# Performance work log

Hardware: AMD Instinct MI355X
Metric: run time of the kernel (lower is better)

The kernel has to match this reference:

```python
import jax, jax.numpy as jnp
import numpy as np

CANVAS = 28
MARGIN = 2
HALF = CANVAS / 2.0          # 14
SCALE = CANVAS / 2.0 - MARGIN  # 12
P = 2        # num_paths
SEG = 4      # final segments
T = 8        # curve samples per bezier segment
AA = 2       # 2x2 = 4 anti-alias subsamples per pixel


def _lin(x, w, b):
    return x @ w + b


def _render(cp, widths, alphas):
    """diffvg-style rasterizer.
    cp: [B,P,S,4,2] cubic bezier control points, widths/alphas: [B,P].
    Returns [B,1,H,W] image over white background (paths paint dark).
    """
    B = cp.shape[0]
    t = jnp.linspace(0.0, 1.0, T)
    mt = 1.0 - t
    basis = jnp.stack([mt**3, 3*mt**2*t, 3*mt*t**2, t**3], axis=1)  # [T,4]
    pts = jnp.einsum('tk,bpskd->bpstd', basis, cp)                   # [B,P,S,T,2]
    q = pts.reshape(B, P, SEG * T, 2)                                # polyline [B,P,M,2]

    # 2x2 subpixel sample grid over the canvas
    Nf = CANVAS * AA
    c = (jnp.arange(Nf, dtype=jnp.float32) + 0.5) / AA               # fine coords
    sy, sx = jnp.meshgrid(c, c, indexing='ij')
    s = jnp.stack([sx.ravel(), sy.ravel()], axis=-1)                 # [Ns,2] (x,y)

    # stroke coverage: distance from each sample to nearest curve sample
    qq = jnp.sum(q * q, axis=-1)                                     # [B,P,M]
    ss = jnp.sum(s * s, axis=-1)                                     # [Ns]
    cr = jnp.einsum('bpmd,nd->bpmn', q, s)                           # [B,P,M,Ns]
    d2 = jnp.maximum(qq[..., None] + ss - 2.0 * cr, 0.0)
    dist = jnp.sqrt(jnp.min(d2, axis=2))                             # [B,P,Ns]
    stroke = jnp.clip(widths[..., None] * 0.5 + 0.5 - dist, 0.0, 1.0)

    # fill coverage: even-odd crossing number on the closed polyline
    qn = jnp.roll(q, -1, axis=2)
    x0, y0 = q[..., 0], q[..., 1]
    x1, y1 = qn[..., 0], qn[..., 1]
    syf, sxf = s[:, 1], s[:, 0]
    crossing_band = (y0[..., None] > syf) != (y1[..., None] > syf)   # [B,P,M,Ns]
    te = (syf - y0[..., None]) / (y1[..., None] - y0[..., None] + 1e-8)
    xint = x0[..., None] + te * (x1 - x0)[..., None]
    ncross = jnp.sum((crossing_band & (sxf < xint)).astype(jnp.int32), axis=2)
    inside = (ncross % 2).astype(dist.dtype)                         # [B,P,Ns]

    cov = jnp.maximum(inside, stroke)
    img = jnp.prod(1.0 - alphas[..., None] * cov, axis=1)            # composite over paths, bg=1
    img = img.reshape(B, CANVAS, AA, CANVAS, AA).mean(axis=(2, 4))   # AA resolve
    return img[:, None]                                              # [B,1,H,W]


def setup_inputs() -> dict:
    key = jax.random.key(0)
    ks = jax.random.split(key, 16)
    def W(k, i, o):
        return jax.random.normal(k, (i, o), jnp.float32) / np.sqrt(i).astype(np.float32)
    B = 128
    return {
        'x': jax.random.uniform(ks[0], (B, 1, 28, 28), jnp.float32),
        'eps': jax.random.normal(ks[1], (B, 64), jnp.float32),
        'enc_w1': W(ks[2], 784, 256), 'enc_b1': jnp.zeros((256,), jnp.float32),
        'enc_w2': W(ks[3], 256, 256), 'enc_b2': jnp.zeros((256,), jnp.float32),
        'mu_w': W(ks[4], 256, 64), 'mu_b': jnp.zeros((64,), jnp.float32),
        'lv_w': W(ks[5], 256, 64), 'lv_b': jnp.zeros((64,), jnp.float32),
        'dec_w1': W(ks[6], 64, 512), 'dec_b1': jnp.zeros((512,), jnp.float32),
        'dec_w2': W(ks[7], 512, 512), 'dec_b2': jnp.zeros((512,), jnp.float32),
        'cp_w': W(ks[8], 512, 28), 'cp_b': jnp.zeros((28,), jnp.float32),
        'ref_w1': W(ks[9], 92, 512), 'ref_b1': jnp.zeros((512,), jnp.float32),
        'ref_w2': W(ks[10], 512, 52), 'ref_b2': jnp.zeros((52,), jnp.float32),
        'wd_w': W(ks[11], 512, 2), 'wd_b': jnp.zeros((2,), jnp.float32),
        'al_w': W(ks[12], 512, 2), 'al_b': jnp.zeros((2,), jnp.float32),
    }


def reference(x, eps, enc_w1, enc_b1, enc_w2, enc_b2, mu_w, mu_b, lv_w, lv_b,
              dec_w1, dec_b1, dec_w2, dec_b2, cp_w, cp_b,
              ref_w1, ref_b1, ref_w2, ref_b2, wd_w, wd_b, al_w, al_b):
    B = x.shape[0]
    # encoder
    h = jax.nn.leaky_relu(_lin(x.reshape(B, -1), enc_w1, enc_b1), 0.2)
    h = jax.nn.leaky_relu(_lin(h, enc_w2, enc_b2), 0.2)
    mu = _lin(h, mu_w, mu_b)
    logvar = _lin(h, lv_w, lv_b)
    z = mu + eps * jnp.exp(0.5 * logvar)
    # hierarchical decoder
    h2 = jax.nn.selu(_lin(jax.nn.selu(_lin(z, dec_w1, dec_b1)), dec_w2, dec_b2))
    coarse = jnp.tanh(_lin(h2, cp_w, cp_b)).reshape(B, P, 7, 2) * SCALE + HALF
    pts_norm = (coarse - HALF) / SCALE
    h_in = jnp.concatenate([z, pts_norm.reshape(B, -1)], axis=-1)
    refined = jnp.tanh(_lin(jax.nn.selu(_lin(h_in, ref_w1, ref_b1)), ref_w2, ref_b2))
    points = refined.reshape(B, P, 13, 2) * SCALE + HALF
    seg_idx = 3 * jnp.arange(SEG)[:, None] + jnp.arange(4)[None, :]  # [S,4]
    control_points = points[:, :, seg_idx, :]                         # [B,P,S,4,2]
    widths = jax.nn.sigmoid(_lin(h2, wd_w, wd_b)) * 2.0 + 1.0
    alphas = jax.nn.sigmoid(_lin(h2, al_w, al_b))
    rendered = 1.0 - _render(control_points, widths, alphas)          # white digit on black
    return (rendered, mu, logvar, control_points, widths, alphas)
```

## Files before the change

kernel.cpp:

```cpp
#include <hip/hip_runtime.h>
#include <math.h>


#define O_MU  100352
#define O_LV  108544
#define O_CP  116736
#define O_WD  124928
#define O_AL  125184

__device__ __forceinline__ float leaky(float x) {
    return x >= 0.0f ? x : 0.2f * x;
}
__device__ __forceinline__ float selu(float x) {
    const float scale = 1.0507009873554805f;
    const float alpha = 1.6732632423543772f;
    return x > 0.0f ? scale * x : scale * (alpha * expm1f(x));
}
__device__ __forceinline__ void fma4(float4& acc, float a, const float4 w) {
    acc.x = fmaf(a, w.x, acc.x);
    acc.y = fmaf(a, w.y, acc.y);
    acc.z = fmaf(a, w.z, acc.z);
    acc.w = fmaf(a, w.w, acc.w);
}
__device__ __forceinline__ void add4(float4& a, const float4 b) {
    a.x += b.x; a.y += b.y; a.z += b.z; a.w += b.w;
}

__global__ __launch_bounds__(512, 1)
void pipeline(const float* __restrict__ x, const float* __restrict__ eps,
              const float* __restrict__ enc_w1, const float* __restrict__ enc_b1,
              const float* __restrict__ enc_w2, const float* __restrict__ enc_b2,
              const float* __restrict__ mu_w, const float* __restrict__ mu_b,
              const float* __restrict__ lv_w, const float* __restrict__ lv_b,
              const float* __restrict__ dec_w1, const float* __restrict__ dec_b1,
              const float* __restrict__ dec_w2, const float* __restrict__ dec_b2,
              const float* __restrict__ cp_w, const float* __restrict__ cp_b,
              const float* __restrict__ ref_w1, const float* __restrict__ ref_b1,
              const float* __restrict__ ref_w2, const float* __restrict__ ref_b2,
              const float* __restrict__ wd_w, const float* __restrict__ wd_b,
              const float* __restrict__ al_w, const float* __restrict__ al_b,
              float* __restrict__ out) {
    __shared__ float  sX[784];
    __shared__ float4 sPart4[512];
    __shared__ float  sH1[256];
    __shared__ float  sHe[256];
    __shared__ float  sML[128];
    __shared__ float  sIn[96];
    __shared__ float  sD1[512];
    __shared__ float  sH2[512];
    __shared__ float  sR1[512];
    __shared__ float  sP[56];
    __shared__ float  sQ[128];
    __shared__ float  sWA[4];

    const int row = blockIdx.x;
    const int tid = threadIdx.x;

    for (int i = tid; i < 784; i += 512) sX[i] = x[row * 784 + i];
    __syncthreads();

    {
        const int jv = tid & 63, g = tid >> 6;
        const float4* __restrict__ W4 = (const float4*)enc_w1;
        const int k0 = g * 98;
        float4 acc0 = {0,0,0,0}, acc1 = {0,0,0,0};
#pragma unroll 7
        for (int i = 0; i < 98; i += 2) {
            fma4(acc0, sX[k0 + i + 0], W4[(k0 + i + 0) * 64 + jv]);
            fma4(acc1, sX[k0 + i + 1], W4[(k0 + i + 1) * 64 + jv]);
        }
        add4(acc0, acc1);
        sPart4[g * 64 + jv] = acc0;
    }
    __syncthreads();
    if (tid < 64) {
        float4 s = ((const float4*)enc_b1)[tid];
#pragma unroll
        for (int g = 0; g < 8; g++) add4(s, sPart4[g * 64 + tid]);
        s.x = leaky(s.x); s.y = leaky(s.y); s.z = leaky(s.z); s.w = leaky(s.w);
        ((float4*)sH1)[tid] = s;
    }
    __syncthreads();

    {
        const int jv = tid & 63, g = tid >> 6;
        const float4* __restrict__ W4 = (const float4*)enc_w2;
        const int k0 = g * 32;
        float4 acc0 = {0,0,0,0}, acc1 = {0,0,0,0};
#pragma unroll 8
        for (int i = 0; i < 32; i += 2) {
            fma4(acc0, sH1[k0 + i + 0], W4[(k0 + i + 0) * 64 + jv]);
            fma4(acc1, sH1[k0 + i + 1], W4[(k0 + i + 1) * 64 + jv]);
        }
        add4(acc0, acc1);
        sPart4[g * 64 + jv] = acc0;
    }
    __syncthreads();
    if (tid < 64) {
        float4 s = ((const float4*)enc_b2)[tid];
#pragma unroll
        for (int g = 0; g < 8; g++) add4(s, sPart4[g * 64 + tid]);
        s.x = leaky(s.x); s.y = leaky(s.y); s.z = leaky(s.z); s.w = leaky(s.w);
        ((float4*)sHe)[tid] = s;
    }
    __syncthreads();

    {
        const int o4 = tid >> 4, g = tid & 15;
        const int jv = o4 & 15;
        const float4* __restrict__ W4 = (const float4*)(o4 < 16 ? mu_w : lv_w);
        const int k0 = g * 16;
        float4 acc = {0,0,0,0};
#pragma unroll
        for (int i = 0; i < 16; i++)
            fma4(acc, sHe[k0 + i], W4[(k0 + i) * 16 + jv]);
        sPart4[o4 * 16 + g] = acc;
    }
    __syncthreads();
    if (tid < 32) {
        const int jv = tid & 15;
        float4 s = (tid < 16) ? ((const float4*)mu_b)[jv] : ((const float4*)lv_b)[jv];
#pragma unroll
        for (int g = 0; g < 16; g++) add4(s, sPart4[tid * 16 + g]);
        ((float4*)sML)[tid] = s;
        float4* o4p = (float4*)(out + (tid < 16 ? O_MU : O_LV) + row * 64);
        o4p[jv] = s;
    }
    __syncthreads();
    if (tid < 64)
        sIn[tid] = fmaf(eps[row * 64 + tid], expf(0.5f * sML[64 + tid]), sML[tid]);
    __syncthreads();

    {
        const int jv = tid & 127, g = tid >> 7;
        const float4* __restrict__ W4 = (const float4*)dec_w1;
        const int k0 = g * 16;
        float4 acc = {0,0,0,0};
#pragma unroll
        for (int i = 0; i < 16; i++)
            fma4(acc, sIn[k0 + i], W4[(k0 + i) * 128 + jv]);
        sPart4[g * 128 + jv] = acc;
    }
    __syncthreads();
    if (tid < 128) {
        float4 s = ((const float4*)dec_b1)[tid];
#pragma unroll
        for (int g = 0; g < 4; g++) add4(s, sPart4[g * 128 + tid]);
        s.x = selu(s.x); s.y = selu(s.y); s.z = selu(s.z); s.w = selu(s.w);
        ((float4*)sD1)[tid] = s;
    }
    __syncthreads();

    {
        const int jv = tid & 127, g = tid >> 7;
        const float4* __restrict__ W4 = (const float4*)dec_w2;
        const int k0 = g * 128;
        float4 acc0 = {0,0,0,0}, acc1 = {0,0,0,0};
        float4 acc2 = {0,0,0,0}, acc3 = {0,0,0,0};
#pragma unroll 4
        for (int i = 0; i < 128; i += 4) {
            fma4(acc0, sD1[k0 + i + 0], W4[(k0 + i + 0) * 128 + jv]);
            fma4(acc1, sD1[k0 + i + 1], W4[(k0 + i + 1) * 128 + jv]);
            fma4(acc2, sD1[k0 + i + 2], W4[(k0 + i + 2) * 128 + jv]);
            fma4(acc3, sD1[k0 + i + 3], W4[(k0 + i + 3) * 128 + jv]);
        }
        add4(acc0, acc1); add4(acc2, acc3); add4(acc0, acc2);
        sPart4[g * 128 + jv] = acc0;
    }
    __syncthreads();
    if (tid < 128) {
        float4 s = ((const float4*)dec_b2)[tid];
#pragma unroll
        for (int g = 0; g < 4; g++) add4(s, sPart4[g * 128 + tid]);
        s.x = selu(s.x); s.y = selu(s.y); s.z = selu(s.z); s.w = selu(s.w);
        ((float4*)sH2)[tid] = s;
    }
    __syncthreads();

    {
        const int o = tid >> 4, g = tid & 15;
        const float* __restrict__ W;
        int ldw, col;
        if (o < 28)      { W = cp_w; ldw = 28; col = o; }
        else if (o < 30) { W = wd_w; ldw = 2;  col = o - 28; }
        else             { W = al_w; ldw = 2;  col = o - 30; }
        float acc = 0.f;
        for (int k = g; k < 512; k += 16) acc = fmaf(sH2[k], W[k * ldw + col], acc);
        acc += __shfl_xor(acc, 1);
        acc += __shfl_xor(acc, 2);
        acc += __shfl_xor(acc, 4);
        acc += __shfl_xor(acc, 8);
        if (g == 0) {
            if (o < 28) {
                sIn[64 + o] = tanhf(acc + cp_b[col]);
            } else if (o < 30) {
                float v = 1.f / (1.f + expf(-(acc + wd_b[col])));
                v = fmaf(v, 2.f, 1.f);
                out[O_WD + row * 2 + col] = v;
                sWA[col] = v;
            } else {
                float v = 1.f / (1.f + expf(-(acc + al_b[col])));
                out[O_AL + row * 2 + col] = v;
                sWA[2 + col] = v;
            }
        }
    }
    __syncthreads();

    {
        const int jv = tid & 127, g = tid >> 7;
        const float4* __restrict__ W4 = (const float4*)ref_w1;
        const int k0 = g * 23;
        float4 acc = {0,0,0,0};
#pragma unroll
        for (int i = 0; i < 23; i++)
            fma4(acc, sIn[k0 + i], W4[(k0 + i) * 128 + jv]);
        sPart4[g * 128 + jv] = acc;
    }
    __syncthreads();
    if (tid < 128) {
        float4 s = ((const float4*)ref_b1)[tid];
#pragma unroll
        for (int g = 0; g < 4; g++) add4(s, sPart4[g * 128 + tid]);
        s.x = selu(s.x); s.y = selu(s.y); s.z = selu(s.z); s.w = selu(s.w);
        ((float4*)sR1)[tid] = s;
    }
    __syncthreads();

    {
        const int o = tid >> 3, g = tid & 7;
        float acc = 0.f;
        if (o < 52)
            for (int k = g; k < 512; k += 8) acc = fmaf(sR1[k], ref_w2[k * 52 + o], acc);
        acc += __shfl_xor(acc, 1);
        acc += __shfl_xor(acc, 2);
        acc += __shfl_xor(acc, 4);
        if (g == 0 && o < 52)
            sP[o] = fmaf(tanhf(acc + ref_b2[o]), 12.f, 14.f);
    }
    __syncthreads();

    if (tid < 64) {
        int idx = tid;
        int p = idx >> 5, rest = idx & 31;
        int s = rest >> 3, kk = (rest >> 1) & 3, d = idx & 1;
        out[O_CP + row * 64 + idx] = sP[p * 26 + (3 * s + kk) * 2 + d];
    }
    if (tid < 128) {
        int idx = tid;
        int p = idx >> 6, s = (idx >> 4) & 3, ti = (idx >> 1) & 7, d = idx & 1;
        float t = (float)ti / 7.0f;
        float mt = 1.0f - t;
        float c0 = mt * mt * mt;
        float c1 = 3.f * mt * mt * t;
        float c2 = 3.f * mt * t * t;
        float c3 = t * t * t;
        const float* base = sP + p * 26 + (3 * s) * 2 + d;
        sQ[idx] = c0 * base[0] + c1 * base[2] + c2 * base[4] + c3 * base[6];
    }
    __syncthreads();

    const float2* __restrict__ sQ2 = (const float2*)sQ;
    for (int u = tid; u < 3136; u += 512) {
        const int pixel = u >> 2;
        const int sub = u & 3;
        const int py = pixel / 28;
        const int px = pixel - py * 28;
        const float sy = ((float)(2 * py + (sub >> 1)) + 0.5f) * 0.5f;
        const float sx = ((float)(2 * px + (sub & 1)) + 0.5f) * 0.5f;
        float img = 1.0f;
#pragma unroll
        for (int p = 0; p < 2; p++) {
            float dmin2 = 1e30f;
            int cnt = 0;
            float2 cur = sQ2[p * 32];
            bool bp = cur.y > sy;
#pragma unroll
            for (int m = 0; m < 32; m++) {
                float2 nxt = sQ2[p * 32 + ((m + 1) & 31)];
                float dx = sx - cur.x;
                float dy = sy - cur.y;
                dmin2 = fminf(dmin2, fmaf(dx, dx, dy * dy));
                bool bn = nxt.y > sy;
                float den = nxt.y - cur.y + 1e-8f;
                float lhs = dx * den;
                float rhs = dy * (nxt.x - cur.x);
                if ((bp != bn) && ((lhs < rhs) == (den > 0.0f))) cnt++;
                cur = nxt;
                bp = bn;
            }
            float dist = sqrtf(dmin2);
            float stroke = fminf(fmaxf(fmaf(sWA[p], 0.5f, 0.5f) - dist, 0.f), 1.f);
            float cov = fmaxf((float)(cnt & 1), stroke);
            img *= fmaf(-sWA[2 + p], cov, 1.0f);
        }
        img += __shfl_xor(img, 1);
        img += __shfl_xor(img, 2);
        if (sub == 0) out[row * 784 + pixel] = 1.0f - 0.25f * img;
    }
}

extern "C" void kernel_launch(void* const* d_in, const int* in_sizes, int n_in,
                              void* d_out, int out_size, void* d_ws, size_t ws_size,
                              hipStream_t stream) {
    const float* x      = (const float*)d_in[0];
    const float* eps    = (const float*)d_in[1];
    const float* enc_w1 = (const float*)d_in[2];
    const float* enc_b1 = (const float*)d_in[3];
    const float* enc_w2 = (const float*)d_in[4];
    const float* enc_b2 = (const float*)d_in[5];
    const float* mu_w   = (const float*)d_in[6];
    const float* mu_b   = (const float*)d_in[7];
    const float* lv_w   = (const float*)d_in[8];
    const float* lv_b   = (const float*)d_in[9];
    const float* dec_w1 = (const float*)d_in[10];
    const float* dec_b1 = (const float*)d_in[11];
    const float* dec_w2 = (const float*)d_in[12];
    const float* dec_b2 = (const float*)d_in[13];
    const float* cp_w   = (const float*)d_in[14];
    const float* cp_b   = (const float*)d_in[15];
    const float* ref_w1 = (const float*)d_in[16];
    const float* ref_b1 = (const float*)d_in[17];
    const float* ref_w2 = (const float*)d_in[18];
    const float* ref_b2 = (const float*)d_in[19];
    const float* wd_w   = (const float*)d_in[20];
    const float* wd_b   = (const float*)d_in[21];
    const float* al_w   = (const float*)d_in[22];
    const float* al_b   = (const float*)d_in[23];

    float* out = (float*)d_out;

    pipeline<<<128, 512, 0, stream>>>(x, eps, enc_w1, enc_b1, enc_w2, enc_b2,
                                      mu_w, mu_b, lv_w, lv_b, dec_w1, dec_b1,
                                      dec_w2, dec_b2, cp_w, cp_b, ref_w1, ref_b1,
                                      ref_w2, ref_b2, wd_w, wd_b, al_w, al_b,
                                      out);
}
```

Baseline: 212.5 us.

## Split fused per-row pipeline into per-layer kernels with column-parallel blocks

Replaces the single 128-block fused kernel with nine kernels, one per MLP layer plus a rasterizer. Each layer kernel assigns output columns and row halves to blocks and keeps activations transposed in a global workspace. The rasterizer splits each image into seven chunks across blocks. The goal is to spread weight reads and raster work over many more CUs than the original 128 blocks used. In exchange it adds kernel launch overhead, global round trips for intermediates, and scalar (non-vectorised) strided weight loads.

Measured after the change: 190.0 us. 10.6% less time.

```diff
diff --git a/kernel.cpp b/kernel.cpp
--- a/kernel.cpp
+++ b/kernel.cpp
@@ -8,266 +8,277 @@
 #define O_WD  124928
 #define O_AL  125184
 
-__device__ __forceinline__ float leaky(float x) {
-    return x >= 0.0f ? x : 0.2f * x;
-}
-__device__ __forceinline__ float selu(float x) {
-    const float scale = 1.0507009873554805f;
-    const float alpha = 1.6732632423543772f;
-    return x > 0.0f ? scale * x : scale * (alpha * expm1f(x));
-}
-__device__ __forceinline__ void fma4(float4& acc, float a, const float4 w) {
-    acc.x = fmaf(a, w.x, acc.x);
-    acc.y = fmaf(a, w.y, acc.y);
-    acc.z = fmaf(a, w.z, acc.z);
-    acc.w = fmaf(a, w.w, acc.w);
-}
-__device__ __forceinline__ void add4(float4& a, const float4 b) {
-    a.x += b.x; a.y += b.y; a.z += b.z; a.w += b.w;
-}
-
-__global__ __launch_bounds__(512, 1)
-void pipeline(const float* __restrict__ x, const float* __restrict__ eps,
-              const float* __restrict__ enc_w1, const float* __restrict__ enc_b1,
-              const float* __restrict__ enc_w2, const float* __restrict__ enc_b2,
-              const float* __restrict__ mu_w, const float* __restrict__ mu_b,
-              const float* __restrict__ lv_w, const float* __restrict__ lv_b,
-              const float* __restrict__ dec_w1, const float* __restrict__ dec_b1,
-              const float* __restrict__ dec_w2, const float* __restrict__ dec_b2,
-              const float* __restrict__ cp_w, const float* __restrict__ cp_b,
-              const float* __restrict__ ref_w1, const float* __restrict__ ref_b1,
-              const float* __restrict__ ref_w2, const float* __restrict__ ref_b2,
-              const float* __restrict__ wd_w, const float* __restrict__ wd_b,
-              const float* __restrict__ al_w, const float* __restrict__ al_b,
+#define W_H1   0
+#define W_HE   32768
+#define W_MUT  65536
+#define W_LVT  73728
+#define W_D1   81920
+#define W_H2   147456
+#define W_PN   212992
+#define W_R1   216576
+#define W_PT   282112
+#define W_WA   288768
+
+__device__ __forceinline__ float leaky(float x) { return x >= 0.f ? x : 0.2f * x; }
+__device__ __forceinline__ float seluf(float x) {
+    const float s = 1.0507009873554805f, a = 1.6732632423543772f;
+    return x > 0.f ? s * x : s * (a * expm1f(x));
+}
+__device__ __forceinline__ float sigm(float x) { return 1.f / (1.f + expf(-x)); }
+
+__global__ __launch_bounds__(512)
+void enc1_k(const float* __restrict__ x, const float* __restrict__ w,
+            const float* __restrict__ b, float* __restrict__ outT) {
+    __shared__ float part[8][64];
+    const int j = blockIdx.x >> 1, h = blockIdx.x & 1;
+    const int tid = threadIdx.x, lane = tid & 63, ks = tid >> 6;
+    const int r = h * 64 + lane;
+    const float* __restrict__ xr = x + r * 784;
+    float acc = 0.f;
+    const int k0 = ks * 98;
+#pragma unroll 7
+    for (int i = 0; i < 98; i++)
+        acc = fmaf(xr[k0 + i], w[(k0 + i) * 256 + j], acc);
+    part[ks][lane] = acc;
+    __syncthreads();
+    if (tid < 64) {
+        float s = b[j];
+#pragma unroll
+        for (int q = 0; q < 8; q++) s += part[q][tid];
+        outT[j * 128 + h * 64 + tid] = leaky(s);
+    }
+}
+
+__global__ __launch_bounds__(512)
+void enc2_k(const float* __restrict__ inT, const float* __restrict__ w,
+            const float* __restrict__ b, float* __restrict__ outT) {
+    __shared__ float part[8][64];
+    const int j = blockIdx.x >> 1, h = blockIdx.x & 1;
+    const int tid = threadIdx.x, lane = tid & 63, ks = tid >> 6;
+    const int r = h * 64 + lane;
+    float acc = 0.f;
+    const int k0 = ks * 32;
+#pragma unroll 8
+    for (int i = 0; i < 32; i++)
+        acc = fmaf(inT[(k0 + i) * 128 + r], w[(k0 + i) * 256 + j], acc);
+    part[ks][lane] = acc;
+    __syncthreads();
+    if (tid < 64) {
+        float s = b[j];
+#pragma unroll
+        for (int q = 0; q < 8; q++) s += part[q][tid];
+        outT[j * 128 + h * 64 + tid] = leaky(s);
+    }
+}
+
+__global__ __launch_bounds__(512)
+void mulv_k(const float* __restrict__ heT,
+            const float* __restrict__ mu_w, const float* __restrict__ mu_b,
+            const float* __restrict__ lv_w, const float* __restrict__ lv_b,
+            float* __restrict__ muT, float* __restrict__ lvT,
+            float* __restrict__ out) {
+    __shared__ float part[8][64];
+    const int meta = blockIdx.x >> 1, h = blockIdx.x & 1;
+    const int head = meta >> 6, col = meta & 63;
+    const float* __restrict__ w = head ? lv_w : mu_w;
+    const int tid = threadIdx.x, lane = tid & 63, ks = tid >> 6;
+    const int r = h * 64 + lane;
+    float acc = 0.f;
+    const int k0 = ks * 32;
+#pragma unroll 8
+    for (int i = 0; i < 32; i++)
+        acc = fmaf(heT[(k0 + i) * 128 + r], w[(k0 + i) * 64 + col], acc);
+    part[ks][lane] = acc;
+    __syncthreads();
+    if (tid < 64) {
+        float s = (head ? lv_b : mu_b)[col];
+#pragma unroll
+        for (int q = 0; q < 8; q++) s += part[q][tid];
+        const int rr = h * 64 + tid;
+        (head ? lvT : muT)[col * 128 + rr] = s;
+        out[(head ? O_LV : O_MU) + rr * 64 + col] = s;
+    }
+}
+
+__global__ __launch_bounds__(512)
+void dec1_k(const float* __restrict__ muT, const float* __restrict__ lvT,
+            const float* __restrict__ eps, const float* __restrict__ w,
+            const float* __restrict__ b, float* __restrict__ outT) {
+    __shared__ float part[8][2][64];
+    const int j0 = (blockIdx.x >> 1) * 2, h = blockIdx.x & 1;
+    const int tid = threadIdx.x, lane = tid & 63, ks = tid >> 6;
+    const int r = h * 64 + lane;
+    float a0 = 0.f, a1 = 0.f;
+    const int k0 = ks * 8;
+#pragma unroll
+    for (int i = 0; i < 8; i++) {
+        const int k = k0 + i;
+        float zv = fmaf(eps[r * 64 + k], expf(0.5f * lvT[k * 128 + r]), muT[k * 128 + r]);
+        a0 = fmaf(zv, w[k * 512 + j0],     a0);
+        a1 = fmaf(zv, w[k * 512 + j0 + 1], a1);
+    }
+    part[ks][0][lane] = a0; part[ks][1][lane] = a1;
+    __syncthreads();
+    if (tid < 128) {
+        const int c = tid >> 6, ll = tid & 63;
+        float s = b[j0 + c];
+#pragma unroll
+        for (int q = 0; q < 8; q++) s += part[q][c][ll];
+        outT[(j0 + c) * 128 + h * 64 + ll] = seluf(s);
+    }
+}
+
+__global__ __launch_bounds__(512)
+void dec2_k(const float* __restrict__ inT, const float* __restrict__ w,
+            const float* __restrict__ b, float* __restrict__ outT) {
+    __shared__ float part[8][2][64];
+    const int j0 = (blockIdx.x >> 1) * 2, h = blockIdx.x & 1;
+    const int tid = threadIdx.x, lane = tid & 63, ks = tid >> 6;
+    const int r = h * 64 + lane;
+    float a0 = 0.f, a1 = 0.f;
+    const int k0 = ks * 64;
+#pragma unroll 4
+    for (int i = 0; i < 64; i++) {
+        const float v = inT[(k0 + i) * 128 + r];
+        a0 = fmaf(v, w[(k0 + i) * 512 + j0],     a0);
+        a1 = fmaf(v, w[(k0 + i) * 512 + j0 + 1], a1);
+    }
+    part[ks][0][lane] = a0; part[ks][1][lane] = a1;
+    __syncthreads();
+    if (tid < 128) {
+        const int c = tid >> 6, ll = tid & 63;
+        float s = b[j0 + c];
+#pragma unroll
+        for (int q = 0; q < 8; q++) s += part[q][c][ll];
+        outT[(j0 + c) * 128 + h * 64 + ll] = seluf(s);
+    }
+}
+
+__global__ __launch_bounds__(512)
+void heads_k(const float* __restrict__ h2T,
+             const float* __restrict__ cp_w, const float* __restrict__ cp_b,
+             const float* __restrict__ wd_w, const float* __restrict__ wd_b,
+             const float* __restrict__ al_w, const float* __restrict__ al_b,
+             float* __restrict__ pnT, float* __restrict__ waT,
+             float* __restrict__ out) {
+    __shared__ float part[8][64];
+    const int j = blockIdx.x >> 1, h = blockIdx.x & 1;
+    const float* __restrict__ w; int ldw, col;
+    if (j < 28)      { w = cp_w; ldw = 28; col = j; }
+    else if (j < 30) { w = wd_w; ldw = 2;  col = j - 28; }
+    else             { w = al_w; ldw = 2;  col = j - 30; }
+    const int tid = threadIdx.x, lane = tid & 63, ks = tid >> 6;
+    const int r = h * 64 + lane;
+    float acc = 0.f;
+    const int k0 = ks * 64;
+#pragma unroll 8
+    for (int i = 0; i < 64; i++)
+        acc = fmaf(h2T[(k0 + i) * 128 + r], w[(k0 + i) * ldw + col], acc);
+    part[ks][lane] = acc;
+    __syncthreads();
+    if (tid < 64) {
+        float s = 0.f;
+#pragma unroll
+        for (int q = 0; q < 8; q++) s += part[q][tid];
+        const int rr = h * 64 + tid;
+        if (j < 28) {
+            pnT[j * 128 + rr] = tanhf(s + cp_b[col]);
+        } else if (j < 30) {
+            float v = fmaf(sigm(s + wd_b[col]), 2.f, 1.f);
+            out[O_WD + rr * 2 + col] = v; waT[col * 128 + rr] = v;
+        } else {
+            float v = sigm(s + al_b[col]);
+            out[O_AL + rr * 2 + col] = v; waT[(2 + col) * 128 + rr] = v;
+        }
+    }
+}
+
+__global__ __launch_bounds__(512)
+void ref1_k(const float* __restrict__ muT, const float* __restrict__ lvT,
+            const float* __restrict__ eps, const float* __restrict__ pnT,
+            const float* __restrict__ w, const float* __restrict__ b,
+            float* __restrict__ outT) {
+    __shared__ float part[8][2][64];
+    const int j0 = (blockIdx.x >> 1) * 2, h = blockIdx.x & 1;
+    const int tid = threadIdx.x, lane = tid & 63, ks = tid >> 6;
+    const int r = h * 64 + lane;
+    float a0 = 0.f, a1 = 0.f;
+#pragma unroll
+    for (int i = 0; i < 12; i++) {
+        const int k = ks * 12 + i;
+        if (k < 92) {
+            float v = (k < 64)
+                ? fmaf(eps[r * 64 + k], expf(0.5f * lvT[k * 128 + r]), muT[k * 128 + r])
+                : pnT[(k - 64) * 128 + r];
+            a0 = fmaf(v, w[k * 512 + j0],     a0);
+            a1 = fmaf(v, w[k * 512 + j0 + 1], a1);
+        }
+    }
+    part[ks][0][lane] = a0; part[ks][1][lane] = a1;
+    __syncthreads();
+    if (tid < 128) {
+        const int c = tid >> 6, ll = tid & 63;
+        float s = b[j0 + c];
+#pragma unroll
+        for (int q = 0; q < 8; q++) s += part[q][c][ll];
+        outT[(j0 + c) * 128 + h * 64 + ll] = seluf(s);
+    }
+}
+
+__global__ __launch_bounds__(512)
+void ref2_k(const float* __restrict__ r1T, const float* __restrict__ w,
+            const float* __restrict__ b, float* __restrict__ PT) {
+    __shared__ float part[8][64];
+    const int j = blockIdx.x >> 1, h = blockIdx.x & 1;
+    const int tid = threadIdx.x, lane = tid & 63, ks = tid >> 6;
+    const int r = h * 64 + lane;
+    float acc = 0.f;
+    const int k0 = ks * 64;
+#pragma unroll 8
+    for (int i = 0; i < 64; i++)
+        acc = fmaf(r1T[(k0 + i) * 128 + r], w[(k0 + i) * 52 + j], acc);
+    part[ks][lane] = acc;
+    __syncthreads();
+    if (tid < 64) {
+        float s = b[j];
+#pragma unroll
+        for (int q = 0; q < 8; q++) s += part[q][tid];
+        PT[j * 128 + h * 64 + tid] = fmaf(tanhf(s), 12.f, 14.f);
+    }
+}
+
+__global__ __launch_bounds__(512)
+void raster_k(const float* __restrict__ PT, const float* __restrict__ waT,
               float* __restrict__ out) {
-    __shared__ float  sX[784];
-    __shared__ float4 sPart4[512];
-    __shared__ float  sH1[256];
-    __shared__ float  sHe[256];
-    __shared__ float  sML[128];
-    __shared__ float  sIn[96];
-    __shared__ float  sD1[512];
-    __shared__ float  sH2[512];
-    __shared__ float  sR1[512];
-    __shared__ float  sP[56];
-    __shared__ float  sQ[128];
-    __shared__ float  sWA[4];
-
-    const int row = blockIdx.x;
+    __shared__ float sP[56];
+    __shared__ float sWA[4];
+    __shared__ float sQ[128];
+    const int bid = blockIdx.x;
+    const int row = bid / 7, chunk = bid - row * 7;
     const int tid = threadIdx.x;
-
-    for (int i = tid; i < 784; i += 512) sX[i] = x[row * 784 + i];
-    __syncthreads();
-
-    {
-        const int jv = tid & 63, g = tid >> 6;
-        const float4* __restrict__ W4 = (const float4*)enc_w1;
-        const int k0 = g * 98;
-        float4 acc0 = {0,0,0,0}, acc1 = {0,0,0,0};
-#pragma unroll 7
-        for (int i = 0; i < 98; i += 2) {
-            fma4(acc0, sX[k0 + i + 0], W4[(k0 + i + 0) * 64 + jv]);
-            fma4(acc1, sX[k0 + i + 1], W4[(k0 + i + 1) * 64 + jv]);
-        }
-        add4(acc0, acc1);
-        sPart4[g * 64 + jv] = acc0;
-    }
-    __syncthreads();
-    if (tid < 64) {
-        float4 s = ((const float4*)enc_b1)[tid];
-#pragma unroll
-        for (int g = 0; g < 8; g++) add4(s, sPart4[g * 64 + tid]);
-        s.x = leaky(s.x); s.y = leaky(s.y); s.z = leaky(s.z); s.w = leaky(s.w);
-        ((float4*)sH1)[tid] = s;
-    }
-    __syncthreads();
-
-    {
-        const int jv = tid & 63, g = tid >> 6;
-        const float4* __restrict__ W4 = (const float4*)enc_w2;
-        const int k0 = g * 32;
-        float4 acc0 = {0,0,0,0}, acc1 = {0,0,0,0};
-#pragma unroll 8
-        for (int i = 0; i < 32; i += 2) {
-            fma4(acc0, sH1[k0 + i + 0], W4[(k0 + i + 0) * 64 + jv]);
-            fma4(acc1, sH1[k0 + i + 1], W4[(k0 + i + 1) * 64 + jv]);
-        }
-        add4(acc0, acc1);
-        sPart4[g * 64 + jv] = acc0;
-    }
-    __syncthreads();
-    if (tid < 64) {
-        float4 s = ((const float4*)enc_b2)[tid];
-#pragma unroll
-        for (int g = 0; g < 8; g++) add4(s, sPart4[g * 64 + tid]);
-        s.x = leaky(s.x); s.y = leaky(s.y); s.z = leaky(s.z); s.w = leaky(s.w);
-        ((float4*)sHe)[tid] = s;
-    }
-    __syncthreads();
-
-    {
-        const int o4 = tid >> 4, g = tid & 15;
-        const int jv = o4 & 15;
-        const float4* __restrict__ W4 = (const float4*)(o4 < 16 ? mu_w : lv_w);
-        const int k0 = g * 16;
-        float4 acc = {0,0,0,0};
-#pragma unroll
-        for (int i = 0; i < 16; i++)
-            fma4(acc, sHe[k0 + i], W4[(k0 + i) * 16 + jv]);
-        sPart4[o4 * 16 + g] = acc;
-    }
-    __syncthreads();
-    if (tid < 32) {
-        const int jv = tid & 15;
-        float4 s = (tid < 16) ? ((const float4*)mu_b)[jv] : ((const float4*)lv_b)[jv];
-#pragma unroll
-        for (int g = 0; g < 16; g++) add4(s, sPart4[tid * 16 + g]);
-        ((float4*)sML)[tid] = s;
-        float4* o4p = (float4*)(out + (tid < 16 ? O_MU : O_LV) + row * 64);
-        o4p[jv] = s;
-    }
-    __syncthreads();
-    if (tid < 64)
-        sIn[tid] = fmaf(eps[row * 64 + tid], expf(0.5f * sML[64 + tid]), sML[tid]);
-    __syncthreads();
-
-    {
-        const int jv = tid & 127, g = tid >> 7;
-        const float4* __restrict__ W4 = (const float4*)dec_w1;
-        const int k0 = g * 16;
-        float4 acc = {0,0,0,0};
-#pragma unroll
-        for (int i = 0; i < 16; i++)
-            fma4(acc, sIn[k0 + i], W4[(k0 + i) * 128 + jv]);
-        sPart4[g * 128 + jv] = acc;
-    }
-    __syncthreads();
+    if (tid < 52) sP[tid] = PT[tid * 128 + row];
+    if (tid >= 64 && tid < 68) sWA[tid - 64] = waT[(tid - 64) * 128 + row];
+    __syncthreads();
+    if (chunk == 0 && tid < 64) {
+        const int idx = tid, p = idx >> 5, rest = idx & 31;
+        const int s = rest >> 3, kk = (rest >> 1) & 3, d = idx & 1;
+        out[O_CP + row * 64 + idx] = sP[p * 26 + (3 * s + kk) * 2 + d];
+    }
     if (tid < 128) {
-        float4 s = ((const float4*)dec_b1)[tid];
-#pragma unroll
-        for (int g = 0; g < 4; g++) add4(s, sPart4[g * 128 + tid]);
-        s.x = selu(s.x); s.y = selu(s.y); s.z = selu(s.z); s.w = selu(s.w);
-        ((float4*)sD1)[tid] = s;
-    }
-    __syncthreads();
-
-    {
-        const int jv = tid & 127, g = tid >> 7;
-        const float4* __restrict__ W4 = (const float4*)dec_w2;
-        const int k0 = g * 128;
-        float4 acc0 = {0,0,0,0}, acc1 = {0,0,0,0};
-        float4 acc2 = {0,0,0,0}, acc3 = {0,0,0,0};
-#pragma unroll 4
-        for (int i = 0; i < 128; i += 4) {
-            fma4(acc0, sD1[k0 + i + 0], W4[(k0 + i + 0) * 128 + jv]);
-            fma4(acc1, sD1[k0 + i + 1], W4[(k0 + i + 1) * 128 + jv]);
-            fma4(acc2, sD1[k0 + i + 2], W4[(k0 + i + 2) * 128 + jv]);
-            fma4(acc3, sD1[k0 + i + 3], W4[(k0 + i + 3) * 128 + jv]);
-        }
-        add4(acc0, acc1); add4(acc2, acc3); add4(acc0, acc2);
-        sPart4[g * 128 + jv] = acc0;
-    }
-    __syncthreads();
-    if (tid < 128) {
-        float4 s = ((const float4*)dec_b2)[tid];
-#pragma unroll
-        for (int g = 0; g < 4; g++) add4(s, sPart4[g * 128 + tid]);
-        s.x = selu(s.x); s.y = selu(s.y); s.z = selu(s.z); s.w = selu(s.w);
-        ((float4*)sH2)[tid] = s;
-    }
-    __syncthreads();
-
-    {
-        const int o = tid >> 4, g = tid & 15;
-        const float* __restrict__ W;
-        int ldw, col;
-        if (o < 28)      { W = cp_w; ldw = 28; col = o; }
-        else if (o < 30) { W = wd_w; ldw = 2;  col = o - 28; }
-        else             { W = al_w; ldw = 2;  col = o - 30; }
-        float acc = 0.f;
-        for (int k = g; k < 512; k += 16) acc = fmaf(sH2[k], W[k * ldw + col], acc);
-        acc += __shfl_xor(acc, 1);
-        acc += __shfl_xor(acc, 2);
-        acc += __shfl_xor(acc, 4);
-        acc += __shfl_xor(acc, 8);
-        if (g == 0) {
-            if (o < 28) {
-                sIn[64 + o] = tanhf(acc + cp_b[col]);
-            } else if (o < 30) {
-                float v = 1.f / (1.f + expf(-(acc + wd_b[col])));
-                v = fmaf(v, 2.f, 1.f);
-                out[O_WD + row * 2 + col] = v;
-                sWA[col] = v;
-            } else {
-                float v = 1.f / (1.f + expf(-(acc + al_b[col])));
-                out[O_AL + row * 2 + col] = v;
-                sWA[2 + col] = v;
-            }
-        }
-    }
-    __syncthreads();
-
-    {
-        const int jv = tid & 127, g = tid >> 7;
-        const float4* __restrict__ W4 = (const float4*)ref_w1;
-        const int k0 = g * 23;
-        float4 acc = {0,0,0,0};
-#pragma unroll
-        for (int i = 0; i < 23; i++)
-            fma4(acc, sIn[k0 + i], W4[(k0 + i) * 128 + jv]);
-        sPart4[g * 128 + jv] = acc;
-    }
-    __syncthreads();
-    if (tid < 128) {
-        float4 s = ((const float4*)ref_b1)[tid];
-#pragma unroll
-        for (int g = 0; g < 4; g++) add4(s, sPart4[g * 128 + tid]);
-        s.x = selu(s.x); s.y = selu(s.y); s.z = selu(s.z); s.w = selu(s.w);
-        ((float4*)sR1)[tid] = s;
-    }
-    __syncthreads();
-
-    {
-        const int o = tid >> 3, g = tid & 7;
-        float acc = 0.f;
-        if (o < 52)
-            for (int k = g; k < 512; k += 8) acc = fmaf(sR1[k], ref_w2[k * 52 + o], acc);
-        acc += __shfl_xor(acc, 1);
-        acc += __shfl_xor(acc, 2);
-        acc += __shfl_xor(acc, 4);
-        if (g == 0 && o < 52)
-            sP[o] = fmaf(tanhf(acc + ref_b2[o]), 12.f, 14.f);
-    }
-    __syncthreads();
-
-    if (tid < 64) {
-        int idx = tid;
-        int p = idx >> 5, rest = idx & 31;
-        int s = rest >> 3, kk = (rest >> 1) & 3, d = idx & 1;
-        out[O_CP + row * 64 + idx] = sP[p * 26 + (3 * s + kk) * 2 + d];
-    }
-    if (tid < 128) {
-        int idx = tid;
-        int p = idx >> 6, s = (idx >> 4) & 3, ti = (idx >> 1) & 7, d = idx & 1;
-        float t = (float)ti / 7.0f;
-        float mt = 1.0f - t;
-        float c0 = mt * mt * mt;
-        float c1 = 3.f * mt * mt * t;
-        float c2 = 3.f * mt * t * t;
-        float c3 = t * t * t;
-        const float* base = sP + p * 26 + (3 * s) * 2 + d;
+        const int idx = tid, p = idx >> 6, s = (idx >> 4) & 3, ti = (idx >> 1) & 7, d = idx & 1;
+        const float t = (float)ti / 7.0f, mt = 1.0f - t;
+        const float c0 = mt * mt * mt, c1 = 3.f * mt * mt * t;
+        const float c2 = 3.f * mt * t * t, c3 = t * t * t;
+        const float* base = sP + p * 26 + 6 * s + d;
         sQ[idx] = c0 * base[0] + c1 * base[2] + c2 * base[4] + c3 * base[6];
     }
     __syncthreads();
-
-    const float2* __restrict__ sQ2 = (const float2*)sQ;
-    for (int u = tid; u < 3136; u += 512) {
-        const int pixel = u >> 2;
-        const int sub = u & 3;
-        const int py = pixel / 28;
-        const int px = pixel - py * 28;
+    if (tid < 448) {
+        const int pixel = chunk * 112 + (tid >> 2), sub = tid & 3;
+        const int py = pixel / 28, px = pixel - py * 28;
         const float sy = ((float)(2 * py + (sub >> 1)) + 0.5f) * 0.5f;
         const float sx = ((float)(2 * px + (sub & 1)) + 0.5f) * 0.5f;
+        const float2* __restrict__ sQ2 = (const float2*)sQ;
         float img = 1.0f;
 #pragma unroll
         for (int p = 0; p < 2; p++) {
@@ -329,10 +340,19 @@
     const float* al_b   = (const float*)d_in[23];
 
     float* out = (float*)d_out;
-
-    pipeline<<<128, 512, 0, stream>>>(x, eps, enc_w1, enc_b1, enc_w2, enc_b2,
-                                      mu_w, mu_b, lv_w, lv_b, dec_w1, dec_b1,
-                                      dec_w2, dec_b2, cp_w, cp_b, ref_w1, ref_b1,
-                                      ref_w2, ref_b2, wd_w, wd_b, al_w, al_b,
-                                      out);
-}
+    float* ws  = (float*)d_ws;
+
+    enc1_k <<<512, 512, 0, stream>>>(x, enc_w1, enc_b1, ws + W_H1);
+    enc2_k <<<512, 512, 0, stream>>>(ws + W_H1, enc_w2, enc_b2, ws + W_HE);
+    mulv_k <<<256, 512, 0, stream>>>(ws + W_HE, mu_w, mu_b, lv_w, lv_b,
+                                     ws + W_MUT, ws + W_LVT, out);
+    dec1_k <<<512, 512, 0, stream>>>(ws + W_MUT, ws + W_LVT, eps,
+                                     dec_w1, dec_b1, ws + W_D1);
+    dec2_k <<<512, 512, 0, stream>>>(ws + W_D1, dec_w2, dec_b2, ws + W_H2);
+    heads_k<<<64, 512, 0, stream>>>(ws + W_H2, cp_w, cp_b, wd_w, wd_b, al_w, al_b,
+                                    ws + W_PN, ws + W_WA, out);
+    ref1_k <<<512, 512, 0, stream>>>(ws + W_MUT, ws + W_LVT, eps, ws + W_PN,
+                                     ref_w1, ref_b1, ws + W_R1);
+    ref2_k <<<104, 512, 0, stream>>>(ws + W_R1, ref_w2, ref_b2, ws + W_PT);
+    raster_k<<<896, 512, 0, stream>>>(ws + W_PT, ws + W_WA, out);
+}
```
